# Optimization experiments

Hardware: AMD Instinct MI355X
Metric: run time of the kernel (lower is better)

## Reference

```python
import jax, jax.numpy as jnp
import numpy as np

D_MODEL = 1024
NUM_HEADS = 16
DEPTH = D_MODEL // NUM_HEADS


def setup_inputs() -> dict:
    key = jax.random.key(0)
    ks = jax.random.split(key, 9)
    B, S = 2, 2048
    scale = 1.0 / np.sqrt(D_MODEL)
    x = jax.random.normal(ks[0], (B, S, D_MODEL), dtype=jnp.float32)
    wq = jax.random.normal(ks[1], (D_MODEL, D_MODEL), dtype=jnp.float32) * scale
    wk = jax.random.normal(ks[2], (D_MODEL, D_MODEL), dtype=jnp.float32) * scale
    wv = jax.random.normal(ks[3], (D_MODEL, D_MODEL), dtype=jnp.float32) * scale
    wo = jax.random.normal(ks[4], (D_MODEL, D_MODEL), dtype=jnp.float32) * scale
    bq = jnp.zeros((D_MODEL,), dtype=jnp.float32)
    bk = jnp.zeros((D_MODEL,), dtype=jnp.float32)
    bv = jnp.zeros((D_MODEL,), dtype=jnp.float32)
    bo = jnp.zeros((D_MODEL,), dtype=jnp.float32)
    return {"x": x, "wq": wq, "bq": bq, "wk": wk, "bk": bk,
            "wv": wv, "bv": bv, "wo": wo, "bo": bo}


def _split_heads(t):
    # [B, S, D] -> [B, H, S, depth]
    B, S, _ = t.shape
    return t.reshape(B, S, NUM_HEADS, DEPTH).transpose(0, 2, 1, 3)


def reference(x, wq, bq, wk, bk, wv, bv, wo, bo):
    q = _split_heads(x @ wq + bq)
    k = _split_heads(x @ wk + bk)
    v = _split_heads(x @ wv + bv)
    # scaled dot-product attention with materialized [B,H,S,S] scores
    logits = jnp.einsum("bhqd,bhkd->bhqk", q, k) / jnp.sqrt(
        jnp.asarray(DEPTH, dtype=x.dtype))
    attn = jax.nn.softmax(logits, axis=-1)
    out = jnp.einsum("bhqk,bhkd->bhqd", attn, v)
    B, _, S, _ = out.shape
    concat = out.transpose(0, 2, 1, 3).reshape(B, S, D_MODEL)
    return concat @ wo + bo
```

## Files before the change

kernel.cpp:

```cpp
#include <hip/hip_runtime.h>
#include <hip/hip_bf16.h>
#include <stdint.h>

typedef unsigned short u16;
typedef __attribute__((ext_vector_type(8))) short short8;
typedef __attribute__((ext_vector_type(4))) short s4v;
typedef __attribute__((ext_vector_type(4))) float f32x4;

__device__ __forceinline__ float bf2f(u16 u) {
    union { uint32_t u; float f; } v; v.u = ((uint32_t)u) << 16; return v.f;
}
__device__ __forceinline__ u16 f2bf(float f) {
    union { float f; uint32_t u; } v; v.f = f;
    uint32_t r = (v.u + 0x7fffu + ((v.u >> 16) & 1u)) >> 16;
    return (u16)r;
}
__device__ __forceinline__ uint32_t pkbf(float a, float b) {
    union { __hip_bfloat162 h; uint32_t w; } u;
    u.h = __float22bfloat162_rn(float2{a, b});
    return u.w;
}
__device__ __forceinline__ void store_out(u16* p, float v) { *p = f2bf(v); }
__device__ __forceinline__ void store_out(float* p, float v) { *p = v; }

__device__ __forceinline__ void async_ld16(const u16* g, u16* l) {
    __builtin_amdgcn_global_load_lds(
        (const __attribute__((address_space(1))) void*)g,
        (__attribute__((address_space(3))) void*)l, 16, 0, 0);
}

__global__ void prep(const float* __restrict__ x,
                     const float* __restrict__ w0, const float* __restrict__ w1,
                     const float* __restrict__ w2,
                     u16* __restrict__ xb, u16* __restrict__ wT) {
    const int z = blockIdx.z;
    __shared__ u16 tile[32][33];
    if (z >= 3) {
        int blk = (z - 3) * 1024 + blockIdx.y * 32 + blockIdx.x;
        int tid = threadIdx.y * 32 + threadIdx.x;
        int i = (blk * 256 + tid) * 8;
        float4 a = *(const float4*)(x + i);
        float4 b = *(const float4*)(x + i + 4);
        union { uint32_t w[4]; uint4 v; } o;
        o.w[0] = pkbf(a.x, a.y); o.w[1] = pkbf(a.z, a.w);
        o.w[2] = pkbf(b.x, b.y); o.w[3] = pkbf(b.z, b.w);
        *(uint4*)(xb + i) = o.v;
        return;
    }
    const float* in = (z == 0) ? w0 : (z == 1) ? w1 : w2;
    u16* o = wT + (size_t)z * 1024 * 1024;
    int xx = blockIdx.x * 32 + threadIdx.x;
    int y0 = blockIdx.y * 32;
#pragma unroll
    for (int j = threadIdx.y; j < 32; j += 8)
        tile[j][threadIdx.x] = f2bf(in[(size_t)(y0 + j) * 1024 + xx]);
    __syncthreads();
    int ox = blockIdx.y * 32 + threadIdx.x;
    int oy0 = blockIdx.x * 32;
#pragma unroll
    for (int j = threadIdx.y; j < 32; j += 8)
        o[(size_t)(oy0 + j) * 1024 + ox] = tile[threadIdx.x][j];
}

__global__ void transpose1(const float* __restrict__ w, u16* __restrict__ out) {
    __shared__ u16 tile[32][33];
    int x = blockIdx.x * 32 + threadIdx.x;
    int y0 = blockIdx.y * 32;
#pragma unroll
    for (int j = threadIdx.y; j < 32; j += 8)
        tile[j][threadIdx.x] = f2bf(w[(size_t)(y0 + j) * 1024 + x]);
    __syncthreads();
    int ox = blockIdx.y * 32 + threadIdx.x;
    int oy0 = blockIdx.x * 32;
#pragma unroll
    for (int j = threadIdx.y; j < 32; j += 8)
        out[(size_t)(oy0 + j) * 1024 + ox] = tile[threadIdx.x][j];
}

#define GBM 128
#define GBN 128
#define GBK 32

template <typename OutT>
__global__ __launch_bounds__(256) void gemm_bt(
    const u16* __restrict__ A, int lda,
    const u16* __restrict__ BT, int ldb,
    const float* __restrict__ bias0, const float* __restrict__ bias1,
    const float* __restrict__ bias2,
    OutT* __restrict__ C, int ldc, int K) {
    __shared__ __align__(16) u16 As[2][GBM * GBK];
    __shared__ __align__(16) u16 Bs[2][GBN * GBK];

    const int tid = threadIdx.x;
    const int wave = tid >> 6, lane = tid & 63;
    const int quad = lane >> 4, l16 = lane & 15;
    const int wr = wave >> 1, wc = wave & 1;
    const int m0 = blockIdx.y * GBM, n0 = blockIdx.x * GBN;

    const int seg = n0 >> 10;
    const float* bsel = (seg == 0) ? bias0 : (seg == 1) ? bias1 : bias2;

    f32x4 acc[4][4] = {};

    const int srow = tid >> 2;
    const int scol = (tid & 3) * 8;
    const u16* Ag0 = A + (size_t)(m0 + srow) * lda + scol;
    const u16* Ag1 = Ag0 + (size_t)64 * lda;
    const u16* Bg0 = BT + (size_t)(n0 + srow) * ldb + scol;
    const u16* Bg1 = Bg0 + (size_t)64 * ldb;
    const int woff = wave << 9;

    async_ld16(Ag0, As[0] + woff);
    async_ld16(Ag1, As[0] + woff + 64 * GBK);
    async_ld16(Bg0, Bs[0] + woff);
    async_ld16(Bg1, Bs[0] + woff + 64 * GBK);

    int cur = 0;
    for (int kb = 0; kb < K; kb += GBK) {
        __syncthreads();

        if (kb + GBK < K) {
            const int nxt = cur ^ 1;
            async_ld16(Ag0 + kb + GBK, As[nxt] + woff);
            async_ld16(Ag1 + kb + GBK, As[nxt] + woff + 64 * GBK);
            async_ld16(Bg0 + kb + GBK, Bs[nxt] + woff);
            async_ld16(Bg1 + kb + GBK, Bs[nxt] + woff + 64 * GBK);
        }

        short8 af[4], bf[4];
#pragma unroll
        for (int mt = 0; mt < 4; mt++)
            af[mt] = *(const short8*)(As[cur] + (wr * 64 + mt * 16 + l16) * GBK + quad * 8);
#pragma unroll
        for (int nt = 0; nt < 4; nt++)
            bf[nt] = *(const short8*)(Bs[cur] + (wc * 64 + nt * 16 + l16) * GBK + quad * 8);
#pragma unroll
        for (int mt = 0; mt < 4; mt++)
#pragma unroll
            for (int nt = 0; nt < 4; nt++)
                acc[mt][nt] = __builtin_amdgcn_mfma_f32_16x16x32_bf16(
                    af[mt], bf[nt], acc[mt][nt], 0, 0, 0);
        cur ^= 1;
    }

#pragma unroll
    for (int nt = 0; nt < 4; nt++) {
        int col = n0 + wc * 64 + nt * 16 + l16;
        float bv = bsel[col & 1023];
#pragma unroll
        for (int mt = 0; mt < 4; mt++) {
            int row = m0 + wr * 64 + mt * 16 + quad * 4;
#pragma unroll
            for (int r = 0; r < 4; r++)
                store_out(&C[(size_t)(row + r) * ldc + col], acc[mt][nt][r] + bv);
        }
    }
}

#define SEQ 2048
#define BQT 128
#define BKV 128
#define LDK 72
#define LDKV 136

__global__ __launch_bounds__(256) void attn(u16* __restrict__ QKV) {
    __shared__ __align__(16) u16 Ks[BKV * LDK];
    __shared__ __align__(16) u16 Vs[64 * LDKV];

    const int tid = threadIdx.x;
    const int wave = tid >> 6, lane = tid & 63;
    const int quad = lane >> 4, l16 = lane & 15;
    const int h = blockIdx.y, bb = blockIdx.z;
    const int q0 = blockIdx.x * BQT;
    const size_t tok0 = (size_t)bb * SEQ;

    const u16* Qb = QKV + tok0 * 3072 + h * 64;
    const u16* Kb = QKV + tok0 * 3072 + 1024 + h * 64;
    const u16* Vb = QKV + tok0 * 3072 + 2048 + h * 64;

    const float cs = 0.18033688011112042f;

    int qr[2];
    qr[0] = q0 + wave * 16 + l16;
    qr[1] = qr[0] + 64;
    short8 aq[2][2];
#pragma unroll
    for (int s = 0; s < 2; s++) {
        union { short8 v; u16 u[8]; uint32_t w[4]; } qa, qb;
        qa.v = *(const short8*)(Qb + (size_t)qr[s] * 3072 + quad * 8);
        qb.v = *(const short8*)(Qb + (size_t)qr[s] * 3072 + 32 + quad * 8);
#pragma unroll
        for (int j = 0; j < 4; j++) {
            qa.w[j] = pkbf(bf2f(qa.u[2 * j]) * cs, bf2f(qa.u[2 * j + 1]) * cs);
            qb.w[j] = pkbf(bf2f(qb.u[2 * j]) * cs, bf2f(qb.u[2 * j + 1]) * cs);
        }
        aq[s][0] = qa.v; aq[s][1] = qb.v;
    }

    float l_i[2] = {0.0f, 0.0f};
    f32x4 o[2][4] = {};

    const int srow = tid >> 2;
    const int scc = (tid & 3) * 16;
    const int pr = tid & 63;
    const int dg = wave;

    const u16* kg = Kb + (size_t)srow * 3072 + scc;
    const u16* vg = Vb + (size_t)(2 * pr) * 3072 + dg * 16;

    uint4 k0r = *(const uint4*)(kg);
    uint4 k1r = *(const uint4*)(kg + 8);
    uint4 k2r = *(const uint4*)(kg + (size_t)64 * 3072);
    uint4 k3r = *(const uint4*)(kg + (size_t)64 * 3072 + 8);
    uint4 va0 = *(const uint4*)(vg);
    uint4 va1 = *(const uint4*)(vg + 8);
    uint4 vb0 = *(const uint4*)(vg + 3072);
    uint4 vb1 = *(const uint4*)(vg + 3072 + 8);

    for (int j0 = 0; j0 < SEQ; j0 += BKV) {
        *(uint4*)(Ks + srow * LDK + scc) = k0r;
        *(uint4*)(Ks + srow * LDK + scc + 8) = k1r;
        *(uint4*)(Ks + (srow + 64) * LDK + scc) = k2r;
        *(uint4*)(Ks + (srow + 64) * LDK + scc + 8) = k3r;
        {
            union { uint4 v[2]; u16 u[16]; } a, b;
            a.v[0] = va0; a.v[1] = va1; b.v[0] = vb0; b.v[1] = vb1;
#pragma unroll
            for (int j = 0; j < 16; j++) {
                uint32_t w = (uint32_t)a.u[j] | ((uint32_t)b.u[j] << 16);
                *(uint32_t*)(Vs + (dg * 16 + j) * LDKV + 2 * pr) = w;
            }
        }
        __syncthreads();

        if (j0 + BKV < SEQ) {
            size_t off = (size_t)(j0 + BKV) * 3072;
            k0r = *(const uint4*)(kg + off);
            k1r = *(const uint4*)(kg + off + 8);
            k2r = *(const uint4*)(kg + off + (size_t)64 * 3072);
            k3r = *(const uint4*)(kg + off + (size_t)64 * 3072 + 8);
            va0 = *(const uint4*)(vg + off);
            va1 = *(const uint4*)(vg + off + 8);
            vb0 = *(const uint4*)(vg + off + 3072);
            vb1 = *(const uint4*)(vg + off + 3072 + 8);
        }

        f32x4 st[2][8];
#pragma unroll
        for (int kkt = 0; kkt < 8; kkt++) {
            f32x4 s0 = {}, s1 = {};
#pragma unroll
            for (int k2 = 0; k2 < 2; k2++) {
                short8 ak = *(const short8*)(Ks + (kkt * 16 + l16) * LDK + k2 * 32 + quad * 8);
                s0 = __builtin_amdgcn_mfma_f32_16x16x32_bf16(ak, aq[0][k2], s0, 0, 0, 0);
                s1 = __builtin_amdgcn_mfma_f32_16x16x32_bf16(ak, aq[1][k2], s1, 0, 0, 0);
            }
            st[0][kkt] = s0; st[1][kkt] = s1;
        }

#pragma unroll
        for (int s = 0; s < 2; s++) {
            float ls = 0.0f;
#pragma unroll
            for (int kkt = 0; kkt < 8; kkt++)
#pragma unroll
                for (int r = 0; r < 4; r++) {
                    st[s][kkt][r] = __builtin_amdgcn_exp2f(st[s][kkt][r]);
                    ls += st[s][kkt][r];
                }
            ls += __shfl_xor(ls, 16, 64);
            ls += __shfl_xor(ls, 32, 64);
            l_i[s] += ls;
        }

#pragma unroll
        for (int kkt = 0; kkt < 8; kkt++) {
            union { uint32_t w[2]; s4v s; } bp0, bp1;
            bp0.w[0] = pkbf(st[0][kkt][0], st[0][kkt][1]);
            bp0.w[1] = pkbf(st[0][kkt][2], st[0][kkt][3]);
            bp1.w[0] = pkbf(st[1][kkt][0], st[1][kkt][1]);
            bp1.w[1] = pkbf(st[1][kkt][2], st[1][kkt][3]);
#pragma unroll
            for (int dt = 0; dt < 4; dt++) {
                s4v av = *(const s4v*)(Vs + (dt * 16 + l16) * LDKV + kkt * 16 + quad * 4);
                o[0][dt] = __builtin_amdgcn_mfma_f32_16x16x16bf16_1k(av, bp0.s, o[0][dt], 0, 0, 0);
                o[1][dt] = __builtin_amdgcn_mfma_f32_16x16x16bf16_1k(av, bp1.s, o[1][dt], 0, 0, 0);
            }
        }

        __syncthreads();
    }

#pragma unroll
    for (int s = 0; s < 2; s++) {
        const float inv_l = 1.0f / l_i[s];
        u16* orow = QKV + (tok0 + qr[s]) * 3072 + h * 64;
#pragma unroll
        for (int dt = 0; dt < 4; dt++) {
            uint32_t w0 = pkbf(o[s][dt][0] * inv_l, o[s][dt][1] * inv_l);
            uint32_t w1 = pkbf(o[s][dt][2] * inv_l, o[s][dt][3] * inv_l);
            uint2 w = {w0, w1};
            *(uint2*)(orow + dt * 16 + quad * 4) = w;
        }
    }
}

extern "C" void kernel_launch(void* const* d_in, const int* in_sizes, int n_in,
                              void* d_out, int out_size, void* d_ws, size_t ws_size,
                              hipStream_t stream) {
    const float* x  = (const float*)d_in[0];
    const float* wq = (const float*)d_in[1];
    const float* bq = (const float*)d_in[2];
    const float* wk = (const float*)d_in[3];
    const float* bk = (const float*)d_in[4];
    const float* wv = (const float*)d_in[5];
    const float* bv = (const float*)d_in[6];
    const float* wo = (const float*)d_in[7];
    const float* bo = (const float*)d_in[8];
    (void)in_sizes; (void)n_in; (void)out_size; (void)ws_size;

    u16* QKV = (u16*)d_ws;
    u16* wT  = QKV + (size_t)4096 * 3072;
    u16* xb  = wT + (size_t)3 * 1024 * 1024;
    u16* woT = xb;

    prep<<<dim3(32, 32, 5), dim3(32, 8), 0, stream>>>(x, wq, wk, wv, xb, wT);
    gemm_bt<u16><<<dim3(24, 32), 256, 0, stream>>>(xb, 1024, wT, 1024, bq, bk, bv,
                                                   QKV, 3072, 1024);
    transpose1<<<dim3(32, 32), dim3(32, 8), 0, stream>>>(wo, woT);
    attn<<<dim3(16, 16, 2), 256, 0, stream>>>(QKV);
    gemm_bt<float><<<dim3(8, 32), 256, 0, stream>>>(QKV, 3072, woT, 1024, bo, bo, bo,
                                                    (float*)d_out, 1024, 1024);
}
```

Baseline: 209.2 us.

## Split attention KV tile across two wave groups with LDS combine

Doubles the attention block to 512 threads. Two groups of four waves each process half of every 128-key tile for the same 128 queries, and their partial outputs and row sums are merged through shared memory at the end. The V tile is stored with a permuted column layout so the PV product can use the 16x16x32 bf16 MFMA instead of 16x16x16. The goal is more waves in flight and lower per-wave latency, at the cost of an extra LDS reduction step and higher register and occupancy pressure from launch_bounds(512,4).

```diff
diff --git a/kernel.cpp b/kernel.cpp
--- a/kernel.cpp
+++ b/kernel.cpp
@@ -163,13 +163,16 @@
 #define LDK 72
 #define LDKV 136
 
-__global__ __launch_bounds__(256) void attn(u16* __restrict__ QKV) {
-    __shared__ __align__(16) u16 Ks[BKV * LDK];
-    __shared__ __align__(16) u16 Vs[64 * LDKV];
+__global__ __launch_bounds__(512, 4) void attn(u16* __restrict__ QKV) {
+    __shared__ __align__(16) u16 SM[BKV * LDK + 64 * LDKV];
+    u16* Ks = SM;
+    u16* Vs = SM + BKV * LDK;
 
     const int tid = threadIdx.x;
     const int wave = tid >> 6, lane = tid & 63;
     const int quad = lane >> 4, l16 = lane & 15;
+    const int wq4 = wave & 3;
+    const int g = wave >> 2;
     const int h = blockIdx.y, bb = blockIdx.z;
     const int q0 = blockIdx.x * BQT;
     const size_t tok0 = (size_t)bb * SEQ;
@@ -181,7 +184,7 @@
     const float cs = 0.18033688011112042f;
 
     int qr[2];
-    qr[0] = q0 + wave * 16 + l16;
+    qr[0] = q0 + wq4 * 16 + l16;
     qr[1] = qr[0] + 64;
     short8 aq[2][2];
 #pragma unroll
@@ -202,33 +205,33 @@
 
     const int srow = tid >> 2;
     const int scc = (tid & 3) * 16;
-    const int pr = tid & 63;
-    const int dg = wave;
-
+    const int pr = lane;
+    const int dgv = wave;
     const u16* kg = Kb + (size_t)srow * 3072 + scc;
-    const u16* vg = Vb + (size_t)(2 * pr) * 3072 + dg * 16;
+    const u16* vg = Vb + (size_t)(2 * pr) * 3072 + dgv * 8;
+
+    const int kvb = 2 * pr;
+    const int kvp = (kvb & 96) | (((kvb >> 2) & 3) << 3) |
+                    (((kvb >> 4) & 1) << 2) | (kvb & 3);
 
     uint4 k0r = *(const uint4*)(kg);
     uint4 k1r = *(const uint4*)(kg + 8);
-    uint4 k2r = *(const uint4*)(kg + (size_t)64 * 3072);
-    uint4 k3r = *(const uint4*)(kg + (size_t)64 * 3072 + 8);
     uint4 va0 = *(const uint4*)(vg);
-    uint4 va1 = *(const uint4*)(vg + 8);
     uint4 vb0 = *(const uint4*)(vg + 3072);
-    uint4 vb1 = *(const uint4*)(vg + 3072 + 8);
+
+    const int kb0 = g * 4;
+    const int t2b = g * 2;
 
     for (int j0 = 0; j0 < SEQ; j0 += BKV) {
         *(uint4*)(Ks + srow * LDK + scc) = k0r;
         *(uint4*)(Ks + srow * LDK + scc + 8) = k1r;
-        *(uint4*)(Ks + (srow + 64) * LDK + scc) = k2r;
-        *(uint4*)(Ks + (srow + 64) * LDK + scc + 8) = k3r;
         {
-            union { uint4 v[2]; u16 u[16]; } a, b;
-            a.v[0] = va0; a.v[1] = va1; b.v[0] = vb0; b.v[1] = vb1;
-#pragma unroll
-            for (int j = 0; j < 16; j++) {
+            union { uint4 v; u16 u[8]; } a, b;
+            a.v = va0; b.v = vb0;
+#pragma unroll
+            for (int j = 0; j < 8; j++) {
                 uint32_t w = (uint32_t)a.u[j] | ((uint32_t)b.u[j] << 16);
-                *(uint32_t*)(Vs + (dg * 16 + j) * LDKV + 2 * pr) = w;
+                *(uint32_t*)(Vs + (dgv * 8 + j) * LDKV + kvp) = w;
             }
         }
         __syncthreads();
@@ -237,36 +240,33 @@
             size_t off = (size_t)(j0 + BKV) * 3072;
             k0r = *(const uint4*)(kg + off);
             k1r = *(const uint4*)(kg + off + 8);
-            k2r = *(const uint4*)(kg + off + (size_t)64 * 3072);
-            k3r = *(const uint4*)(kg + off + (size_t)64 * 3072 + 8);
             va0 = *(const uint4*)(vg + off);
-            va1 = *(const uint4*)(vg + off + 8);
             vb0 = *(const uint4*)(vg + off + 3072);
-            vb1 = *(const uint4*)(vg + off + 3072 + 8);
-        }
-
-        f32x4 st[2][8];
-#pragma unroll
-        for (int kkt = 0; kkt < 8; kkt++) {
+        }
+
+        f32x4 st[2][4];
+#pragma unroll
+        for (int kk = 0; kk < 4; kk++) {
             f32x4 s0 = {}, s1 = {};
 #pragma unroll
             for (int k2 = 0; k2 < 2; k2++) {
-                short8 ak = *(const short8*)(Ks + (kkt * 16 + l16) * LDK + k2 * 32 + quad * 8);
+                short8 ak = *(const short8*)(Ks + ((kb0 + kk) * 16 + l16) * LDK +
+                                             k2 * 32 + quad * 8);
                 s0 = __builtin_amdgcn_mfma_f32_16x16x32_bf16(ak, aq[0][k2], s0, 0, 0, 0);
                 s1 = __builtin_amdgcn_mfma_f32_16x16x32_bf16(ak, aq[1][k2], s1, 0, 0, 0);
             }
-            st[0][kkt] = s0; st[1][kkt] = s1;
+            st[0][kk] = s0; st[1][kk] = s1;
         }
 
 #pragma unroll
         for (int s = 0; s < 2; s++) {
             float ls = 0.0f;
 #pragma unroll
-            for (int kkt = 0; kkt < 8; kkt++)
+            for (int kk = 0; kk < 4; kk++)
 #pragma unroll
                 for (int r = 0; r < 4; r++) {
-                    st[s][kkt][r] = __builtin_amdgcn_exp2f(st[s][kkt][r]);
-                    ls += st[s][kkt][r];
+                    st[s][kk][r] = __builtin_amdgcn_exp2f(st[s][kk][r]);
+                    ls += st[s][kk][r];
                 }
             ls += __shfl_xor(ls, 16, 64);
             ls += __shfl_xor(ls, 32, 64);
@@ -274,33 +274,58 @@
         }
 
 #pragma unroll
-        for (int kkt = 0; kkt < 8; kkt++) {
-            union { uint32_t w[2]; s4v s; } bp0, bp1;
-            bp0.w[0] = pkbf(st[0][kkt][0], st[0][kkt][1]);
-            bp0.w[1] = pkbf(st[0][kkt][2], st[0][kkt][3]);
-            bp1.w[0] = pkbf(st[1][kkt][0], st[1][kkt][1]);
-            bp1.w[1] = pkbf(st[1][kkt][2], st[1][kkt][3]);
+        for (int tt = 0; tt < 2; tt++) {
+            union { uint32_t w[4]; short8 v; } bp0, bp1;
+            bp0.w[0] = pkbf(st[0][2 * tt][0], st[0][2 * tt][1]);
+            bp0.w[1] = pkbf(st[0][2 * tt][2], st[0][2 * tt][3]);
+            bp0.w[2] = pkbf(st[0][2 * tt + 1][0], st[0][2 * tt + 1][1]);
+            bp0.w[3] = pkbf(st[0][2 * tt + 1][2], st[0][2 * tt + 1][3]);
+            bp1.w[0] = pkbf(st[1][2 * tt][0], st[1][2 * tt][1]);
+            bp1.w[1] = pkbf(st[1][2 * tt][2], st[1][2 * tt][3]);
+            bp1.w[2] = pkbf(st[1][2 * tt + 1][0], st[1][2 * tt + 1][1]);
+            bp1.w[3] = pkbf(st[1][2 * tt + 1][2], st[1][2 * tt + 1][3]);
 #pragma unroll
             for (int dt = 0; dt < 4; dt++) {
-                s4v av = *(const s4v*)(Vs + (dt * 16 + l16) * LDKV + kkt * 16 + quad * 4);
-                o[0][dt] = __builtin_amdgcn_mfma_f32_16x16x16bf16_1k(av, bp0.s, o[0][dt], 0, 0, 0);
-                o[1][dt] = __builtin_amdgcn_mfma_f32_16x16x16bf16_1k(av, bp1.s, o[1][dt], 0, 0, 0);
+                short8 av = *(const short8*)(Vs + (dt * 16 + l16) * LDKV +
+                                             (t2b + tt) * 32 + quad * 8);
+                o[0][dt] = __builtin_amdgcn_mfma_f32_16x16x32_bf16(av, bp0.v, o[0][dt], 0, 0, 0);
+                o[1][dt] = __builtin_amdgcn_mfma_f32_16x16x32_bf16(av, bp1.v, o[1][dt], 0, 0, 0);
             }
         }
 
         __syncthreads();
     }
 
-#pragma unroll
-    for (int s = 0; s < 2; s++) {
-        const float inv_l = 1.0f / l_i[s];
-        u16* orow = QKV + (tok0 + qr[s]) * 3072 + h * 64;
-#pragma unroll
-        for (int dt = 0; dt < 4; dt++) {
-            uint32_t w0 = pkbf(o[s][dt][0] * inv_l, o[s][dt][1] * inv_l);
-            uint32_t w1 = pkbf(o[s][dt][2] * inv_l, o[s][dt][3] * inv_l);
-            uint2 w = {w0, w1};
-            *(uint2*)(orow + dt * 16 + quad * 4) = w;
+    float* combO = (float*)SM;
+    float* combL = (float*)SM + 256 * 32;
+    const int slot = wq4 * 64 + lane;
+    if (g == 1) {
+        f32x4* p = (f32x4*)(combO + slot * 32);
+#pragma unroll
+        for (int s = 0; s < 2; s++)
+#pragma unroll
+            for (int dt = 0; dt < 4; dt++)
+                p[s * 4 + dt] = o[s][dt];
+        combL[slot * 2] = l_i[0];
+        combL[slot * 2 + 1] = l_i[1];
+    }
+    __syncthreads();
+    if (g == 0) {
+        const f32x4* p = (const f32x4*)(combO + slot * 32);
+#pragma unroll
+        for (int s = 0; s < 2; s++) {
+            const float inv_l = 1.0f / (l_i[s] + combL[slot * 2 + s]);
+            u16* orow = QKV + (tok0 + qr[s]) * 3072 + h * 64;
+#pragma unroll
+            for (int dt = 0; dt < 4; dt++) {
+                f32x4 ov = p[s * 4 + dt];
+                uint32_t w0 = pkbf((o[s][dt][0] + ov[0]) * inv_l,
+                                   (o[s][dt][1] + ov[1]) * inv_l);
+                uint32_t w1 = pkbf((o[s][dt][2] + ov[2]) * inv_l,
+                                   (o[s][dt][3] + ov[3]) * inv_l);
+                uint2 w = {w0, w1};
+                *(uint2*)(orow + dt * 16 + quad * 4) = w;
+            }
         }
     }
 }
@@ -328,7 +353,7 @@
     gemm_bt<u16><<<dim3(24, 32), 256, 0, stream>>>(xb, 1024, wT, 1024, bq, bk, bv,
                                                    QKV, 3072, 1024);
     transpose1<<<dim3(32, 32), dim3(32, 8), 0, stream>>>(wo, woT);
-    attn<<<dim3(16, 16, 2), 256, 0, stream>>>(QKV);
+    attn<<<dim3(16, 16, 2), 512, 0, stream>>>(QKV);
     gemm_bt<float><<<dim3(8, 32), 256, 0, stream>>>(QKV, 3072, woT, 1024, bo, bo, bo,
                                                     (float*)d_out, 1024, 1024);
 }
```

New measurement: 223.3 us. 1.07x slower.

## Use 16x16x32 MFMA for PV with permuted V layout and MFMA row-sum

Applied to the files above, without the earlier changes.

Replaces the 16x16x16 bf16 MFMAs in the P·V product with 16x16x32 MFMAs, permuting the V columns as they are written to shared memory so each lane's 8-element K slice matches the packed P fragment. It also drops the scalar softmax-denominator accumulation and cross-lane shuffles, computing the row sum with an extra MFMA against a vector of ones. This halves the MFMA instruction count for PV and removes VALU adds and shuffles. In exchange it adds two MFMAs per tile, and the denominator is now summed from bf16-rounded P values.

```diff
diff --git a/kernel.cpp b/kernel.cpp
--- a/kernel.cpp
+++ b/kernel.cpp
@@ -197,8 +197,11 @@
         aq[s][0] = qa.v; aq[s][1] = qb.v;
     }
 
-    float l_i[2] = {0.0f, 0.0f};
     f32x4 o[2][4] = {};
+    f32x4 o_l[2] = {};
+
+    const short8 vone = {16256, 16256, 16256, 16256,
+                         16256, 16256, 16256, 16256};
 
     const int srow = tid >> 2;
     const int scc = (tid & 3) * 16;
@@ -207,6 +210,10 @@
 
     const u16* kg = Kb + (size_t)srow * 3072 + scc;
     const u16* vg = Vb + (size_t)(2 * pr) * 3072 + dg * 16;
+
+    const int kvb = 2 * pr;
+    const int kvp = (kvb & 96) | (((kvb >> 2) & 3) << 3) |
+                    (((kvb >> 4) & 1) << 2) | (kvb & 3);
 
     uint4 k0r = *(const uint4*)(kg);
     uint4 k1r = *(const uint4*)(kg + 8);
@@ -228,7 +235,7 @@
 #pragma unroll
             for (int j = 0; j < 16; j++) {
                 uint32_t w = (uint32_t)a.u[j] | ((uint32_t)b.u[j] << 16);
-                *(uint32_t*)(Vs + (dg * 16 + j) * LDKV + 2 * pr) = w;
+                *(uint32_t*)(Vs + (dg * 16 + j) * LDKV + kvp) = w;
             }
         }
         __syncthreads();
@@ -259,32 +266,33 @@
         }
 
 #pragma unroll
-        for (int s = 0; s < 2; s++) {
-            float ls = 0.0f;
+        for (int s = 0; s < 2; s++)
 #pragma unroll
             for (int kkt = 0; kkt < 8; kkt++)
 #pragma unroll
-                for (int r = 0; r < 4; r++) {
+                for (int r = 0; r < 4; r++)
                     st[s][kkt][r] = __builtin_amdgcn_exp2f(st[s][kkt][r]);
-                    ls += st[s][kkt][r];
-                }
-            ls += __shfl_xor(ls, 16, 64);
-            ls += __shfl_xor(ls, 32, 64);
-            l_i[s] += ls;
-        }
-
-#pragma unroll
-        for (int kkt = 0; kkt < 8; kkt++) {
-            union { uint32_t w[2]; s4v s; } bp0, bp1;
-            bp0.w[0] = pkbf(st[0][kkt][0], st[0][kkt][1]);
-            bp0.w[1] = pkbf(st[0][kkt][2], st[0][kkt][3]);
-            bp1.w[0] = pkbf(st[1][kkt][0], st[1][kkt][1]);
-            bp1.w[1] = pkbf(st[1][kkt][2], st[1][kkt][3]);
+
+#pragma unroll
+        for (int tt = 0; tt < 4; tt++) {
+            union { uint32_t w[4]; short8 v; } bp0, bp1;
+            bp0.w[0] = pkbf(st[0][2 * tt][0], st[0][2 * tt][1]);
+            bp0.w[1] = pkbf(st[0][2 * tt][2], st[0][2 * tt][3]);
+            bp0.w[2] = pkbf(st[0][2 * tt + 1][0], st[0][2 * tt + 1][1]);
+            bp0.w[3] = pkbf(st[0][2 * tt + 1][2], st[0][2 * tt + 1][3]);
+            bp1.w[0] = pkbf(st[1][2 * tt][0], st[1][2 * tt][1]);
+            bp1.w[1] = pkbf(st[1][2 * tt][2], st[1][2 * tt][3]);
+            bp1.w[2] = pkbf(st[1][2 * tt + 1][0], st[1][2 * tt + 1][1]);
+            bp1.w[3] = pkbf(st[1][2 * tt + 1][2], st[1][2 * tt + 1][3]);
+
+            o_l[0] = __builtin_amdgcn_mfma_f32_16x16x32_bf16(vone, bp0.v, o_l[0], 0, 0, 0);
+            o_l[1] = __builtin_amdgcn_mfma_f32_16x16x32_bf16(vone, bp1.v, o_l[1], 0, 0, 0);
 #pragma unroll
             for (int dt = 0; dt < 4; dt++) {
-                s4v av = *(const s4v*)(Vs + (dt * 16 + l16) * LDKV + kkt * 16 + quad * 4);
-                o[0][dt] = __builtin_amdgcn_mfma_f32_16x16x16bf16_1k(av, bp0.s, o[0][dt], 0, 0, 0);
-                o[1][dt] = __builtin_amdgcn_mfma_f32_16x16x16bf16_1k(av, bp1.s, o[1][dt], 0, 0, 0);
+                short8 av = *(const short8*)(Vs + (dt * 16 + l16) * LDKV +
+                                             tt * 32 + quad * 8);
+                o[0][dt] = __builtin_amdgcn_mfma_f32_16x16x32_bf16(av, bp0.v, o[0][dt], 0, 0, 0);
+                o[1][dt] = __builtin_amdgcn_mfma_f32_16x16x32_bf16(av, bp1.v, o[1][dt], 0, 0, 0);
             }
         }
 
@@ -293,7 +301,7 @@
 
 #pragma unroll
     for (int s = 0; s < 2; s++) {
-        const float inv_l = 1.0f / l_i[s];
+        const float inv_l = 1.0f / o_l[s][0];
         u16* orow = QKV + (tok0 + qr[s]) * 3072 + h * 64;
 #pragma unroll
         for (int dt = 0; dt < 4; dt++) {
```

Result: no change. 205.7 us (-1.7%).
